# Optimization experiments

Measured on AMD Instinct MI355X. Metric: run time of the kernel, lower is better.

## Reference

```python
import jax, jax.numpy as jnp
import numpy as np

TWO_PI = np.float32(2.0 * np.pi)
N_GABORS = 256
H = W = 512


def setup_inputs() -> dict:
    key = jax.random.key(0)
    ks = jax.random.split(key, 10)
    f32 = jnp.float32
    return {
        "grid_x": jax.random.uniform(ks[0], (H, W), dtype=f32),
        "grid_y": jax.random.uniform(ks[1], (H, W), dtype=f32),
        "u": jax.random.normal(ks[2], (N_GABORS,), dtype=f32),
        "v": jax.random.normal(ks[3], (N_GABORS,), dtype=f32),
        "theta": 2.0 * jax.random.normal(ks[4], (N_GABORS,), dtype=f32),
        "rel_sigma": 0.05 + 0.7 * jax.random.normal(ks[5], (N_GABORS,), dtype=f32),
        "rel_freq": 0.03 + 5.0 * jax.random.normal(ks[6], (N_GABORS,), dtype=f32),
        "gamma": 0.03 + 0.15 * jax.random.normal(ks[7], (N_GABORS,), dtype=f32),
        "psi": 3.0 * jax.random.normal(ks[8], (N_GABORS, 3), dtype=f32),
        "amplitude": 0.2 * jax.random.normal(ks[9], (N_GABORS, 3), dtype=f32),
    }


def reference(grid_x, grid_y, u, v, theta, rel_sigma, rel_freq, gamma, psi, amplitude):
    # Parameter range enforcement (enforce_parameter_ranges + forward clamps)
    uc = jnp.clip(u, -1.0, 1.0)
    vc = jnp.clip(v, -1.0, 1.0)
    th = jnp.clip(theta, -2.0, 2.0) * TWO_PI           # [N]
    sig = jnp.clip(rel_sigma, 1e-5, 5.0)               # [N]
    gam = jnp.clip(gamma, 1e-5, 5.0)                   # [N]
    psi_c = jnp.clip(psi, -1.0, 1.0)                   # [N,3]
    amp = jnp.clip(amplitude, 0.0, 1.0)                # [N,3]

    cr = jnp.cos(th)[:, None, None]
    sr = jnp.sin(th)[:, None, None]
    dx = grid_x[None, :, :] - uc[:, None, None]        # [N,H,W]
    dy = grid_y[None, :, :] - vc[:, None, None]
    x_rot = dx * cr + dy * sr                          # [N,H,W]
    y_rot = -dx * sr + dy * cr

    gaussian = jnp.exp(jnp.clip(
        -x_rot ** 2 / (2.0 * sig[:, None, None] ** 2)
        - y_rot ** 2 / (2.0 * gam[:, None, None] ** 2),
        -80.0, 80.0))                                  # [N,H,W]

    freq = TWO_PI / jnp.exp(rel_freq)                  # [N]
    phase = psi_c * TWO_PI                             # [N,3]
    fx = freq[:, None, None] * x_rot                   # [N,H,W]

    # cos(fx + phase) = cos(fx)cos(phase) - sin(fx)sin(phase):
    # contract the gabor dim without materializing [N,3,H,W].
    gc = gaussian * jnp.cos(fx)                        # [N,H,W]
    gs = gaussian * jnp.sin(fx)                        # [N,H,W]
    result = (jnp.einsum('nhw,nc->chw', gc, amp * jnp.cos(phase))
              - jnp.einsum('nhw,nc->chw', gs, amp * jnp.sin(phase)))  # [3,H,W]
    return jnp.clip(result, -1.0, 1.0)
```

## Files before the change

kernel.cpp:

```cpp
#include <hip/hip_runtime.h>
#include <stdint.h>

#define NG 256
#define HW (512*512)
#define NCELL 1024
#define CAP 384
#define SPILL_CAP 4096
#define NBIN 256
#define PXB (HW/NBIN)
#define TWO_PI_F 6.283185307179586f
#define L2E 1.4426950408889634f
#define INV2PI_D 0.15915494309189535

static __device__ __forceinline__ float clampf(float x, float lo, float hi) {
    return fminf(fmaxf(x, lo), hi);
}

static __device__ __forceinline__ void compute_consts(
    int n,
    const float* __restrict__ u, const float* __restrict__ v,
    const float* __restrict__ theta, const float* __restrict__ rel_sigma,
    const float* __restrict__ rel_freq, const float* __restrict__ gamma,
    const float* __restrict__ psi, const float* __restrict__ amplitude,
    float4& A, float4& B, float4& C, float4& D)
{
    const float uc = clampf(u[n], -1.f, 1.f);
    const float vc = clampf(v[n], -1.f, 1.f);
    const float th = clampf(theta[n], -2.f, 2.f) * TWO_PI_F;
    const float sg = clampf(rel_sigma[n], 1e-5f, 5.f);
    const float gm = clampf(gamma[n], 1e-5f, 5.f);
    const float cr = (float)::cos((double)th);
    const float sr = (float)::sin((double)th);
    const float i2s = 1.0f / (2.0f * sg * sg);
    const float i2g = 1.0f / (2.0f * gm * gm);
    const float E  = (float)::exp((double)rel_freq[n]);
    const float fq = TWO_PI_F / E;
    A = make_float4(uc, vc, cr, sr);
    B = make_float4(-(i2s * L2E), -(i2g * L2E), fq, 0.f);
    float ac[3], as[3];
    #pragma unroll
    for (int c = 0; c < 3; ++c) {
        const float ph = clampf(psi[n*3 + c], -1.f, 1.f) * TWO_PI_F;
        const float a  = clampf(amplitude[n*3 + c], 0.f, 1.f);
        ac[c] = a * (float)::cos((double)ph);
        as[c] = a * (float)::sin((double)ph);
    }
    C = make_float4(ac[0], ac[1], ac[2], 0.f);
    D = make_float4(as[0], as[1], as[2], 0.f);
}

static __device__ __forceinline__ void accum_list(
    const float4* __restrict__ base, int ngab,
    float gx, float gy, float& a0, float& a1, float& a2)
{
    const float c1f = 0.15915494309189535f;
    const float c2f = (float)(INV2PI_D - (double)0.15915494309189535f);
    for (int j = 0; j < ngab; ++j) {
        const float4 k0 = base[j];
        const float4 k1 = base[NG + j];
        const float dx = gx - k0.x;
        const float dy = gy - k0.y;
        float xr, yr;
        {
            #pragma clang fp contract(off)
            xr = dx * k0.z + dy * k0.w;
            yr = dy * k0.z - dx * k0.w;
        }
        const float e2 = fmaf(yr * yr, k1.y, xr * xr * k1.x);
        if (e2 > -20.0f) {
            const float g = __builtin_amdgcn_exp2f(e2);
            float fx;
            {
                #pragma clang fp contract(off)
                fx = k1.z * xr;
            }
            const float nn = __builtin_rintf(fx * c1f);
            float t = __builtin_fmaf(fx, c1f, -nn);
            t = __builtin_fmaf(fx, c2f, t);
            const float s = __builtin_amdgcn_sinf(t);
            const float c = __builtin_amdgcn_cosf(t);
            const float4 k2 = base[2*NG + j];
            const float4 k3 = base[3*NG + j];
            const float gc = g * c, gs = g * s;
            a0 = fmaf(gc, k2.x, fmaf(-gs, k3.x, a0));
            a1 = fmaf(gc, k2.y, fmaf(-gs, k3.y, a1));
            a2 = fmaf(gc, k2.z, fmaf(-gs, k3.z, a2));
        }
    }
}

__global__ __launch_bounds__(256) void gabor_bin_consts(
    const float* __restrict__ grid_x, const float* __restrict__ grid_y,
    const float* __restrict__ u, const float* __restrict__ v,
    const float* __restrict__ theta, const float* __restrict__ rel_sigma,
    const float* __restrict__ rel_freq, const float* __restrict__ gamma,
    const float* __restrict__ psi, const float* __restrict__ amplitude,
    float4* __restrict__ consts, int* __restrict__ counts,
    float4* __restrict__ bpx,
    int* __restrict__ spill, int* __restrict__ spilln)
{
    const int tid = threadIdx.x;
    if (blockIdx.x == NBIN) {
        float4 A, B, C, D;
        compute_consts(tid, u, v, theta, rel_sigma, rel_freq, gamma, psi,
                       amplitude, A, B, C, D);
        consts[tid] = A; consts[NG+tid] = B;
        consts[2*NG+tid] = C; consts[3*NG+tid] = D;
        return;
    }
    __shared__ int hist[NCELL];
    __shared__ int base[NCELL];
    #pragma unroll
    for (int i = 0; i < NCELL/256; ++i) hist[i*256 + tid] = 0;
    __syncthreads();

    uint32_t rec[PXB/256];
    float px[PXB/256], py[PXB/256];
    const int p0 = blockIdx.x * PXB;
    #pragma unroll
    for (int i = 0; i < PXB/256; ++i) {
        const int p = p0 + i*256 + tid;
        const float x = grid_x[p], y = grid_y[p];
        px[i] = x; py[i] = y;
        int ix = (int)(x * 32.0f); ix = min(max(ix, 0), 31);
        int iy = (int)(y * 32.0f); iy = min(max(iy, 0), 31);
        const int cell = iy*32 + ix;
        const int lr = atomicAdd(&hist[cell], 1);
        rec[i] = ((uint32_t)cell << 11) | (uint32_t)lr;
    }
    __syncthreads();
    #pragma unroll
    for (int i = 0; i < NCELL/256; ++i) {
        const int c = i*256 + tid;
        const int h = hist[c];
        base[c] = (h > 0) ? atomicAdd(&counts[c], h) : 0;
    }
    __syncthreads();
    #pragma unroll
    for (int i = 0; i < PXB/256; ++i) {
        const int p = p0 + i*256 + tid;
        const int cell = (int)(rec[i] >> 11);
        const int g = base[cell] + (int)(rec[i] & 0x7FFu);
        if (g < CAP) {
            bpx[cell*CAP + g] =
                make_float4(__int_as_float(p), px[i], py[i], 0.f);
        } else {
            const int t2 = atomicAdd(spilln, 1);
            if (t2 < SPILL_CAP) spill[t2] = p;
        }
    }
}

__global__ __launch_bounds__(256) void gabor_render(
    const float4* __restrict__ consts, const int* __restrict__ counts,
    const float4* __restrict__ bpx,
    const int* __restrict__ spill, const int* __restrict__ spilln,
    const float* __restrict__ grid_x, const float* __restrict__ grid_y,
    float* __restrict__ out)
{
    __shared__ float4 cs[4 * NG];
    __shared__ int s_wb[4];
    const int cell = blockIdx.x;
    const int tid = threadIdx.x;
    const float cxc = ((cell & 31) + 0.5f) * 0.03125f;
    const float cyc = ((cell >> 5) + 0.5f) * 0.03125f;

    {
        const float4 A = consts[tid];
        const float4 B = consts[NG + tid];
        const float4 C = consts[2*NG + tid];
        const float4 D = consts[3*NG + tid];
        const float dx = cxc - A.x, dy = cyc - A.y;
        const float xrc = dx * A.z + dy * A.w;
        const float yrc = dy * A.z - dx * A.w;
        const float R = 0.0222f;
        const float xl = fmaxf(fabsf(xrc) - R, 0.f);
        const float yl = fmaxf(fabsf(yrc) - R, 0.f);
        const float e2max = xl*xl*B.x + yl*yl*B.y;
        const bool nz = (C.x != 0.f) | (C.y != 0.f) | (C.z != 0.f) |
                        (D.x != 0.f) | (D.y != 0.f) | (D.z != 0.f);
        const bool act = (e2max > -20.0f) && nz;
        const unsigned long long m = __ballot(act);
        const int lane = tid & 63, w = tid >> 6;
        if (lane == 0) s_wb[w] = __popcll(m);
        __syncthreads();
        int base = 0;
        #pragma unroll
        for (int i = 0; i < 4; ++i) base += (i < w) ? s_wb[i] : 0;
        if (act) {
            const int pos = base + __popcll(m & ((1ull << lane) - 1ull));
            cs[pos] = A; cs[NG+pos] = B; cs[2*NG+pos] = C; cs[3*NG+pos] = D;
        }
        __syncthreads();
    }
    const int ng = s_wb[0] + s_wb[1] + s_wb[2] + s_wb[3];

    const float c1f = 0.15915494309189535f;
    const float c2f = (float)(INV2PI_D - (double)0.15915494309189535f);
    const int cnt = min(counts[cell], CAP);
    const int sb = cell * CAP;
    for (int i = tid; i < cnt; i += 256) {
        const float4 pxk = bpx[sb + i];
        const int   p  = __float_as_int(pxk.x);
        const float gx = pxk.y, gy = pxk.z;
        float a0 = 0.f, a1 = 0.f, a2 = 0.f;
        #pragma unroll 2
        for (int j = 0; j < ng; ++j) {
            const float4 k0 = cs[j];
            const float4 k1 = cs[NG + j];
            const float dx = gx - k0.x;
            const float dy = gy - k0.y;
            float xr, yr;
            {
                #pragma clang fp contract(off)
                xr = dx * k0.z + dy * k0.w;
                yr = dy * k0.z - dx * k0.w;
            }
            const float e2 = fmaf(yr * yr, k1.y, xr * xr * k1.x);
            if (e2 > -20.0f) {
                const float g = __builtin_amdgcn_exp2f(e2);
                float fx;
                {
                    #pragma clang fp contract(off)
                    fx = k1.z * xr;
                }
                const float nn = __builtin_rintf(fx * c1f);
                float t = __builtin_fmaf(fx, c1f, -nn);
                t = __builtin_fmaf(fx, c2f, t);
                const float s = __builtin_amdgcn_sinf(t);
                const float c = __builtin_amdgcn_cosf(t);
                const float4 k2 = cs[2*NG + j];
                const float4 k3 = cs[3*NG + j];
                const float gc = g * c, gs = g * s;
                a0 = fmaf(gc, k2.x, fmaf(-gs, k3.x, a0));
                a1 = fmaf(gc, k2.y, fmaf(-gs, k3.y, a1));
                a2 = fmaf(gc, k2.z, fmaf(-gs, k3.z, a2));
            }
        }
        out[p]        = clampf(a0, -1.f, 1.f);
        out[HW + p]   = clampf(a1, -1.f, 1.f);
        out[2*HW + p] = clampf(a2, -1.f, 1.f);
    }

    if (cell == 0) {
        const int sc = min(*spilln, SPILL_CAP);
        for (int i = tid; i < sc; i += 256) {
            const int p = spill[i];
            const float gx = grid_x[p], gy = grid_y[p];
            float a0 = 0.f, a1 = 0.f, a2 = 0.f;
            accum_list(consts, NG, gx, gy, a0, a1, a2);
            out[p]        = clampf(a0, -1.f, 1.f);
            out[HW + p]   = clampf(a1, -1.f, 1.f);
            out[2*HW + p] = clampf(a2, -1.f, 1.f);
        }
    }
}

__global__ __launch_bounds__(256) void gabor_consts_kernel(
    const float* __restrict__ u, const float* __restrict__ v,
    const float* __restrict__ theta, const float* __restrict__ rel_sigma,
    const float* __restrict__ rel_freq, const float* __restrict__ gamma,
    const float* __restrict__ psi, const float* __restrict__ amplitude,
    float4* __restrict__ ws)
{
    const int n = threadIdx.x;
    float4 A, B, C, D;
    compute_consts(n, u, v, theta, rel_sigma, rel_freq, gamma, psi, amplitude,
                   A, B, C, D);
    ws[n] = A; ws[NG + n] = B; ws[2*NG + n] = C; ws[3*NG + n] = D;
}

__global__ __launch_bounds__(256) void gabor_fwd_ws(
    const float4* __restrict__ ws,
    const float* __restrict__ grid_x, const float* __restrict__ grid_y,
    float* __restrict__ out)
{
    __shared__ float4 cs[4 * NG];
    const int tid = threadIdx.x;
    cs[tid]        = ws[tid];
    cs[tid + NG]   = ws[tid + NG];
    cs[tid + 2*NG] = ws[tid + 2*NG];
    cs[tid + 3*NG] = ws[tid + 3*NG];
    __syncthreads();
    const int p = blockIdx.x * 256 + tid;
    const float gx = grid_x[p], gy = grid_y[p];
    float a0 = 0.f, a1 = 0.f, a2 = 0.f;
    accum_list(cs, NG, gx, gy, a0, a1, a2);
    out[p]        = clampf(a0, -1.f, 1.f);
    out[HW + p]   = clampf(a1, -1.f, 1.f);
    out[2*HW + p] = clampf(a2, -1.f, 1.f);
}

__global__ __launch_bounds__(256) void gabor_fwd_fused(
    const float* __restrict__ grid_x, const float* __restrict__ grid_y,
    const float* __restrict__ u, const float* __restrict__ v,
    const float* __restrict__ theta, const float* __restrict__ rel_sigma,
    const float* __restrict__ rel_freq, const float* __restrict__ gamma,
    const float* __restrict__ psi, const float* __restrict__ amplitude,
    float* __restrict__ out)
{
    __shared__ float4 cs[4 * NG];
    const int tid = threadIdx.x;
    {
        float4 A, B, C, D;
        compute_consts(tid, u, v, theta, rel_sigma, rel_freq, gamma, psi,
                       amplitude, A, B, C, D);
        cs[tid] = A; cs[tid + NG] = B; cs[tid + 2*NG] = C; cs[tid + 3*NG] = D;
    }
    __syncthreads();
    const int p = blockIdx.x * 256 + tid;
    const float gx = grid_x[p], gy = grid_y[p];
    float a0 = 0.f, a1 = 0.f, a2 = 0.f;
    accum_list(cs, NG, gx, gy, a0, a1, a2);
    out[p]        = clampf(a0, -1.f, 1.f);
    out[HW + p]   = clampf(a1, -1.f, 1.f);
    out[2*HW + p] = clampf(a2, -1.f, 1.f);
}

extern "C" void kernel_launch(void* const* d_in, const int* in_sizes, int n_in,
                              void* d_out, int out_size, void* d_ws, size_t ws_size,
                              hipStream_t stream) {
    const float* grid_x    = (const float*)d_in[0];
    const float* grid_y    = (const float*)d_in[1];
    const float* u         = (const float*)d_in[2];
    const float* v         = (const float*)d_in[3];
    const float* theta     = (const float*)d_in[4];
    const float* rel_sigma = (const float*)d_in[5];
    const float* rel_freq  = (const float*)d_in[6];
    const float* gamma     = (const float*)d_in[7];
    const float* psi       = (const float*)d_in[8];
    const float* amplitude = (const float*)d_in[9];
    float* out = (float*)d_out;

    const size_t OFF_CONSTS = 0;
    const size_t OFF_COUNTS = 16384;
    const size_t OFF_SPN    = 20480;
    const size_t OFF_SPILL  = 20736;
    const size_t OFF_BPX    = 37120;
    const size_t NEED       = 6328576;

    char* w = (char*)d_ws;

    if (ws_size >= NEED) {
        float4* consts = (float4*)(w + OFF_CONSTS);
        int*    counts = (int*)(w + OFF_COUNTS);
        int*    spn    = (int*)(w + OFF_SPN);
        int*    spill  = (int*)(w + OFF_SPILL);
        float4* bpx    = (float4*)(w + OFF_BPX);

        hipMemsetAsync(w + OFF_COUNTS, 0, 4096 + 256, stream);
        gabor_bin_consts<<<NBIN + 1, 256, 0, stream>>>(
            grid_x, grid_y, u, v, theta, rel_sigma, rel_freq, gamma,
            psi, amplitude, consts, counts, bpx, spill, spn);
        gabor_render<<<NCELL, 256, 0, stream>>>(
            consts, counts, bpx, spill, spn, grid_x, grid_y, out);
    } else if (ws_size >= 4u * NG * sizeof(float4)) {
        float4* ws = (float4*)d_ws;
        gabor_consts_kernel<<<1, NG, 0, stream>>>(
            u, v, theta, rel_sigma, rel_freq, gamma, psi, amplitude, ws);
        gabor_fwd_ws<<<HW / 256, 256, 0, stream>>>(ws, grid_x, grid_y, out);
    } else {
        gabor_fwd_fused<<<HW / 256, 256, 0, stream>>>(
            grid_x, grid_y, u, v, theta, rel_sigma, rel_freq, gamma,
            psi, amplitude, out);
    }
}
```

Baseline: 38.09 us.

## Pack two pixels per thread with v2f math and split gabor list across block halves

Each thread now processes two pixels using 2-wide float vectors, so packed FMA/mul instructions can be used, and the per-cell gabor list is split between the two halves of the block, with partial sums reduced through shared memory. The per-gabor skip branch is removed in the inner loop, so every gabor is evaluated without divergence, and the culling threshold is tightened from -20 to -16. This trades extra exp/sin/cos work on skipped terms and two block barriers per iteration for packed ALU throughput and better balance when pixel counts are low. The tighter threshold slightly changes accuracy near the Gaussian tail.

```diff
diff --git a/kernel.cpp b/kernel.cpp
--- a/kernel.cpp
+++ b/kernel.cpp
@@ -11,10 +11,14 @@
 #define TWO_PI_F 6.283185307179586f
 #define L2E 1.4426950408889634f
 #define INV2PI_D 0.15915494309189535
+#define SKIP_THR (-16.0f)
+
+typedef float v2f __attribute__((ext_vector_type(2)));
 
 static __device__ __forceinline__ float clampf(float x, float lo, float hi) {
     return fminf(fmaxf(x, lo), hi);
 }
+static __device__ __forceinline__ v2f splat(float x) { return (v2f){x, x}; }
 
 static __device__ __forceinline__ void compute_consts(
     int n,
@@ -67,7 +71,7 @@
             yr = dy * k0.z - dx * k0.w;
         }
         const float e2 = fmaf(yr * yr, k1.y, xr * xr * k1.x);
-        if (e2 > -20.0f) {
+        if (e2 > SKIP_THR) {
             const float g = __builtin_amdgcn_exp2f(e2);
             float fx;
             {
@@ -158,8 +162,10 @@
     const float* __restrict__ grid_x, const float* __restrict__ grid_y,
     float* __restrict__ out)
 {
-    __shared__ float4 cs[4 * NG];
+    __shared__ float4 csA[NG], csB[NG], csC[NG], csD[NG];
+    __shared__ float  red[128 * 6];
     __shared__ int s_wb[4];
+
     const int cell = blockIdx.x;
     const int tid = threadIdx.x;
     const float cxc = ((cell & 31) + 0.5f) * 0.03125f;
@@ -179,67 +185,103 @@
         const float e2max = xl*xl*B.x + yl*yl*B.y;
         const bool nz = (C.x != 0.f) | (C.y != 0.f) | (C.z != 0.f) |
                         (D.x != 0.f) | (D.y != 0.f) | (D.z != 0.f);
-        const bool act = (e2max > -20.0f) && nz;
+        const bool act = (e2max > SKIP_THR) && nz;
         const unsigned long long m = __ballot(act);
         const int lane = tid & 63, w = tid >> 6;
         if (lane == 0) s_wb[w] = __popcll(m);
         __syncthreads();
-        int base = 0;
+        int b = 0;
         #pragma unroll
-        for (int i = 0; i < 4; ++i) base += (i < w) ? s_wb[i] : 0;
+        for (int i = 0; i < 4; ++i) b += (i < w) ? s_wb[i] : 0;
         if (act) {
-            const int pos = base + __popcll(m & ((1ull << lane) - 1ull));
-            cs[pos] = A; cs[NG+pos] = B; cs[2*NG+pos] = C; cs[3*NG+pos] = D;
+            const int pos = b + __popcll(m & ((1ull << lane) - 1ull));
+            csA[pos] = A; csB[pos] = B; csC[pos] = C; csD[pos] = D;
         }
         __syncthreads();
     }
-    const int ng = s_wb[0] + s_wb[1] + s_wb[2] + s_wb[3];
+    const int n1 = s_wb[0] + s_wb[1] + s_wb[2] + s_wb[3];
+    const int split = n1 >> 1;
+    const int half = tid >> 7;
+    const int l128 = tid & 127;
+    const int ja = half ? split : 0;
+    const int jb = half ? n1    : split;
 
     const float c1f = 0.15915494309189535f;
     const float c2f = (float)(INV2PI_D - (double)0.15915494309189535f);
+    const v2f c1p = {c1f, c1f};
+    const v2f c2p = {c2f, c2f};
     const int cnt = min(counts[cell], CAP);
     const int sb = cell * CAP;
-    for (int i = tid; i < cnt; i += 256) {
-        const float4 pxk = bpx[sb + i];
-        const int   p  = __float_as_int(pxk.x);
-        const float gx = pxk.y, gy = pxk.z;
-        float a0 = 0.f, a1 = 0.f, a2 = 0.f;
-        #pragma unroll 2
-        for (int j = 0; j < ng; ++j) {
-            const float4 k0 = cs[j];
-            const float4 k1 = cs[NG + j];
-            const float dx = gx - k0.x;
-            const float dy = gy - k0.y;
-            float xr, yr;
-            {
-                #pragma clang fp contract(off)
-                xr = dx * k0.z + dy * k0.w;
-                yr = dy * k0.z - dx * k0.w;
-            }
-            const float e2 = fmaf(yr * yr, k1.y, xr * xr * k1.x);
-            if (e2 > -20.0f) {
-                const float g = __builtin_amdgcn_exp2f(e2);
-                float fx;
+    const int iters = (cnt + 255) >> 8;
+    for (int k = 0; k < iters; ++k) {
+        const int i0 = k*256 + 2*l128;
+        const int i1 = i0 + 1;
+        const bool h0 = i0 < cnt;
+        const bool h1 = i1 < cnt;
+        int p0 = 0, p1 = 0;
+        v2f A0 = {0.f, 0.f}, A1 = {0.f, 0.f}, A2 = {0.f, 0.f};
+        if (h0) {
+            const float4 e0 = bpx[sb + i0];
+            const float4 e1 = h1 ? bpx[sb + i1] : e0;
+            p0 = __float_as_int(e0.x);
+            p1 = __float_as_int(e1.x);
+            const v2f gxp = {e0.y, e1.y};
+            const v2f gyp = {e0.z, e1.z};
+            for (int j = ja; j < jb; ++j) {
+                const float4 k0 = csA[j];
+                const float4 k1 = csB[j];
+                const v2f dx = gxp - splat(k0.x);
+                const v2f dy = gyp - splat(k0.y);
+                v2f xr, yr;
                 {
                     #pragma clang fp contract(off)
-                    fx = k1.z * xr;
+                    xr = dx * splat(k0.z) + dy * splat(k0.w);
+                    yr = dy * splat(k0.z) - dx * splat(k0.w);
                 }
-                const float nn = __builtin_rintf(fx * c1f);
-                float t = __builtin_fmaf(fx, c1f, -nn);
-                t = __builtin_fmaf(fx, c2f, t);
-                const float s = __builtin_amdgcn_sinf(t);
-                const float c = __builtin_amdgcn_cosf(t);
-                const float4 k2 = cs[2*NG + j];
-                const float4 k3 = cs[3*NG + j];
-                const float gc = g * c, gs = g * s;
-                a0 = fmaf(gc, k2.x, fmaf(-gs, k3.x, a0));
-                a1 = fmaf(gc, k2.y, fmaf(-gs, k3.y, a1));
-                a2 = fmaf(gc, k2.z, fmaf(-gs, k3.z, a2));
+                const v2f e2 = (xr * xr) * splat(k1.x) + (yr * yr) * splat(k1.y);
+                const v2f g = { __builtin_amdgcn_exp2f(e2.x),
+                                __builtin_amdgcn_exp2f(e2.y) };
+                v2f fx;
+                {
+                    #pragma clang fp contract(off)
+                    fx = splat(k1.z) * xr;
+                }
+                const v2f r1 = fx * c1p;
+                const v2f nn = { __builtin_rintf(r1.x), __builtin_rintf(r1.y) };
+                v2f t = __builtin_elementwise_fma(fx, c1p, -nn);
+                t = __builtin_elementwise_fma(fx, c2p, t);
+                const v2f s = { __builtin_amdgcn_sinf(t.x),
+                                __builtin_amdgcn_sinf(t.y) };
+                const v2f c = { __builtin_amdgcn_cosf(t.x),
+                                __builtin_amdgcn_cosf(t.y) };
+                const v2f gc = g * c, gs = g * s;
+                const float4 k2 = csC[j];
+                const float4 k3 = csD[j];
+                A0 = __builtin_elementwise_fma(gc, splat(k2.x),
+                     __builtin_elementwise_fma(-gs, splat(k3.x), A0));
+                A1 = __builtin_elementwise_fma(gc, splat(k2.y),
+                     __builtin_elementwise_fma(-gs, splat(k3.y), A1));
+                A2 = __builtin_elementwise_fma(gc, splat(k2.z),
+                     __builtin_elementwise_fma(-gs, splat(k3.z), A2));
             }
         }
-        out[p]        = clampf(a0, -1.f, 1.f);
-        out[HW + p]   = clampf(a1, -1.f, 1.f);
-        out[2*HW + p] = clampf(a2, -1.f, 1.f);
+        __syncthreads();
+        if (half && h0) {
+            red[l128*6 + 0] = A0.x; red[l128*6 + 1] = A1.x;
+            red[l128*6 + 2] = A2.x; red[l128*6 + 3] = A0.y;
+            red[l128*6 + 4] = A1.y; red[l128*6 + 5] = A2.y;
+        }
+        __syncthreads();
+        if (!half && h0) {
+            out[p0]        = clampf(A0.x + red[l128*6 + 0], -1.f, 1.f);
+            out[HW + p0]   = clampf(A1.x + red[l128*6 + 1], -1.f, 1.f);
+            out[2*HW + p0] = clampf(A2.x + red[l128*6 + 2], -1.f, 1.f);
+            if (h1) {
+                out[p1]        = clampf(A0.y + red[l128*6 + 3], -1.f, 1.f);
+                out[HW + p1]   = clampf(A1.y + red[l128*6 + 4], -1.f, 1.f);
+                out[2*HW + p1] = clampf(A2.y + red[l128*6 + 5], -1.f, 1.f);
+            }
+        }
     }
 
     if (cell == 0) {
```

New measurement: 35.56 us. 1.07x faster.
